# Kernel tuning notes

Measured on AMD Instinct MI355X. Metric: run time of the kernel, lower is better.

The kernel has to match this reference:

```python
import jax, jax.numpy as jnp
import numpy as np

B, T, N = 256, 512, 128
GO, EOS = 1, 2  # mead-baseline Offsets
NEG = -10000.0


def setup_inputs() -> dict:
    key = jax.random.key(0)
    k1, k2, k3 = jax.random.split(key, 3)
    unaries = jax.random.normal(k1, (B, T, N), dtype=jnp.float32)
    # constraint mask: True where transition is INVALID (masked to -1e4)
    cmask = jax.random.bernoulli(k2, 0.3, (1, N, N))
    trans = jax.nn.log_softmax(
        jnp.where(cmask, jnp.float32(NEG), jnp.float32(0.0)), axis=1
    )  # [1, N, N], matches buffer construction in __init__
    lengths = jax.random.randint(k3, (B,), T // 2, T + 1).astype(jnp.int64)
    lengths = lengths.at[0].set(T)  # ensure max(lengths) == T
    return {"unaries": unaries, "trans": trans, "lengths": lengths}


def _viterbi(probv, trans, lengths, start_idx, end_idx):
    # probv: [T, B, N] log-probs; trans: [1, N, N]; lengths: [B]
    seq_len, batch, n_tags = probv.shape
    trans0 = trans[0]  # [N(cur), N(prev)]
    lengths = lengths.astype(jnp.int32)

    alphas = jnp.full((batch, n_tags), NEG, probv.dtype).at[:, start_idx].set(0.0)
    alphas = jax.nn.log_softmax(alphas, axis=-1)

    def step(alphas, xs):
        unary_t, i = xs  # [B, N], scalar
        ntv = alphas[:, None, :] + trans0[None]          # [B, N_cur, N_prev]
        bp = jnp.argmax(ntv, axis=2)                     # backpointers [B, N]
        new_alphas = jnp.max(ntv, axis=2) + unary_t      # [B, N]
        alphas = jnp.where((i < lengths)[:, None], new_alphas, alphas)
        return alphas, bp

    alphas, bps = jax.lax.scan(step, alphas, (probv, jnp.arange(seq_len)))

    terminal = alphas + trans0[end_idx][None, :]         # [B, N]
    path_score = jnp.max(terminal, axis=1)               # [B]
    best_tag = jnp.argmax(terminal, axis=1)              # [B]

    rev_len = seq_len - lengths - 1

    def back(btid, xs):
        bp, i = xs  # bp: [B, N]
        new = jnp.take_along_axis(bp, btid[:, None], axis=1)[:, 0]
        btid = jnp.where(i > rev_len, new, btid)
        return btid, btid

    _, ys = jax.lax.scan(back, best_tag, (bps[::-1], jnp.arange(seq_len)))
    full = jnp.concatenate([best_tag[None], ys], axis=0)  # [T+1, B]
    best_path = full[:seq_len][::-1]                       # [T, B]

    seq_mask = jnp.arange(seq_len)[:, None] < lengths[None, :]  # [T, B]
    best_path = jnp.where(seq_mask, best_path, 0)
    return best_path, path_score


def reference(unaries, trans, lengths):
    # constrained branch of TaggerGreedyDecoder.forward (batch_first=True)
    probv = jax.nn.log_softmax(jnp.swapaxes(unaries, 0, 1), axis=-1)  # [T,B,N]
    preds_tb, scores = _viterbi(probv, trans, lengths, GO, EOS)
    return jnp.swapaxes(preds_tb, 0, 1), scores  # ([B,T], [B])
```

## Files before the change

### kernel.cpp

```cpp
#include <hip/hip_runtime.h>

#define BB 256
#define TT 512
#define NN 128
#define GO_IDX 1
#define EOS_IDX 2
#define TSPLIT 368
#define NEGV (-10000.0f)
#define ASLOT(x) ((x) + (((x) >> 5) << 2))

#define STEP_BARRIER() asm volatile("s_waitcnt lgkmcnt(0)\n\ts_barrier" ::: "memory")

typedef float f32x2 __attribute__((ext_vector_type(2)));

__device__ __forceinline__ f32x2 pk_add(f32x2 a, f32x2 b) {
    f32x2 d;
    asm("v_pk_add_f32 %0, %1, %2" : "=v"(d) : "v"(a), "v"(b));
    return d;
}

__device__ __forceinline__ float dpp_xor1_f(float x) {
    return __int_as_float(__builtin_amdgcn_update_dpp(0, __float_as_int(x), 0xB1, 0xF, 0xF, true));
}
__device__ __forceinline__ float dpp_xor2_f(float x) {
    return __int_as_float(__builtin_amdgcn_update_dpp(0, __float_as_int(x), 0x4E, 0xF, 0xF, true));
}
__device__ __forceinline__ int dpp_xor1_i(int x) {
    return __builtin_amdgcn_update_dpp(0, x, 0xB1, 0xF, 0xF, true);
}
__device__ __forceinline__ int dpp_xor2_i(int x) {
    return __builtin_amdgcn_update_dpp(0, x, 0x4E, 0xF, 0xF, true);
}

template <int USE_WS>
__global__ __launch_bounds__(512, 2) void viterbi_kernel(
    float* __restrict__ u,
    const float* __restrict__ trans,
    const int*   __restrict__ lengths_raw,
    float* __restrict__ out,
    unsigned char* __restrict__ ws)
{
    __shared__ unsigned char bps[(TSPLIT - 1) * NN];
    __shared__ __align__(16) float prob[2][16][NN];
    __shared__ __align__(16) float alpha[2][144];
    __shared__ float fin_v[2];
    __shared__ int   fin_i[2];

    const int tid  = threadIdx.x;
    const int b    = blockIdx.x;
    const int wave = tid >> 6;
    const int lane = tid & 63;
    const int q    = tid & 3;
    const int cur  = tid >> 2;
    const int hw   = tid >> 5;
    const int l32  = tid & 31;

    int len;
    {
        int probe = lengths_raw[1];
        len = (probe == 0) ? lengths_raw[2 * b] : lengths_raw[b];
    }

    float* pb = u + (size_t)b * TT * NN;
    const float4* pb4 = (const float4*)pb;
    unsigned char* spb = USE_WS ? (ws + (size_t)b * ((TT - TSPLIT) * NN)) : (unsigned char*)pb;

    f32x2 tr2[16];
    {
        const float4* t4 = (const float4*)(trans + cur * NN + q * 32);
#pragma unroll
        for (int i = 0; i < 8; ++i) {
            float4 v = t4[i];
            f32x2 lo; lo.x = v.x; lo.y = v.y;
            f32x2 hi; hi.x = v.z; hi.y = v.w;
            tr2[2 * i]     = lo;
            tr2[2 * i + 1] = hi;
        }
    }

    if (tid < NN) alpha[0][ASLOT(tid)] = (tid == GO_IDX) ? 0.0f : NEGV;

    auto normrow = [&](float4 v, float* dstrow) {
        float m = fmaxf(fmaxf(v.x, v.y), fmaxf(v.z, v.w));
#pragma unroll
        for (int off = 16; off; off >>= 1) m = fmaxf(m, __shfl_xor(m, off, 64));
        float s = expf(v.x - m) + expf(v.y - m) + expf(v.z - m) + expf(v.w - m);
#pragma unroll
        for (int off = 16; off; off >>= 1) s += __shfl_xor(s, off, 64);
        float ls = logf(s);
        ((float4*)dstrow)[l32] =
            make_float4((v.x - m) - ls, (v.y - m) - ls, (v.z - m) - ls, (v.w - m) - ls);
    };

    float4 R = pb4[hw * 32 + l32];
    normrow(R, &prob[0][hw][0]);
    R = pb4[(16 + hw) * 32 + l32];
    __syncthreads();

    const int nG = (len + 15) >> 4;
    for (int g = 0; g < nG; ++g) {
        const int tb = g << 4;
        normrow(R, &prob[(g + 1) & 1][hw][0]);
        {
            int rr = tb + 32 + hw;
            if (rr > TT - 1) rr = TT - 1;
            R = pb4[rr * 32 + l32];
        }
#pragma unroll 4
        for (int k = 0; k < 16; ++k) {
            const int t = tb + k;
            if (t < len) {
                const float Pv = prob[g & 1][k][cur];
                const float* ra = alpha[t & 1];
                float*       wa = alpha[(t & 1) ^ 1];
                const float4* a4 = (const float4*)(ra + q * 36);
                float bv[4]; int bi4[4];
#pragma unroll
                for (int c = 0; c < 4; ++c) {
                    float4 a0 = a4[c * 2], a1 = a4[c * 2 + 1];
                    f32x2 p0; p0.x = a0.x; p0.y = a0.y;
                    f32x2 p1; p1.x = a0.z; p1.y = a0.w;
                    f32x2 p2; p2.x = a1.x; p2.y = a1.y;
                    f32x2 p3; p3.x = a1.z; p3.y = a1.w;
                    f32x2 s0 = pk_add(p0, tr2[c * 4 + 0]);
                    f32x2 s1 = pk_add(p1, tr2[c * 4 + 1]);
                    f32x2 s2 = pk_add(p2, tr2[c * 4 + 2]);
                    f32x2 s3 = pk_add(p3, tr2[c * 4 + 3]);
                    const int base = c * 8;
                    bv[c] = s0.x; bi4[c] = base + 0;
                    float x;
                    x = s0.y; if (x > bv[c]) { bv[c] = x; bi4[c] = base + 1; }
                    x = s1.x; if (x > bv[c]) { bv[c] = x; bi4[c] = base + 2; }
                    x = s1.y; if (x > bv[c]) { bv[c] = x; bi4[c] = base + 3; }
                    x = s2.x; if (x > bv[c]) { bv[c] = x; bi4[c] = base + 4; }
                    x = s2.y; if (x > bv[c]) { bv[c] = x; bi4[c] = base + 5; }
                    x = s3.x; if (x > bv[c]) { bv[c] = x; bi4[c] = base + 6; }
                    x = s3.y; if (x > bv[c]) { bv[c] = x; bi4[c] = base + 7; }
                }
                float best = bv[0]; int bp = bi4[0];
#pragma unroll
                for (int c = 1; c < 4; ++c) { if (bv[c] > best) { best = bv[c]; bp = bi4[c]; } }
                bp += q * 32;

                float v1 = dpp_xor1_f(best);
                bool  t1 = (q & 1) ? (v1 >= best) : (v1 > best);
                float m1 = t1 ? v1 : best;
                float v2 = dpp_xor2_f(m1);
                bool  t2 = (q & 2) ? (v2 >= m1) : (v2 > m1);
                float M  = t2 ? v2 : m1;

                if (q == 0) wa[ASLOT(cur)] = M + Pv;

                int b1 = dpp_xor1_i(bp);
                int p1i = t1 ? b1 : bp;
                int b2 = dpp_xor2_i(p1i);
                int BP = t2 ? b2 : p1i;

                if (q == 0 && t >= 1) {
                    if (t < TSPLIT) bps[(t - 1) * NN + cur] = (unsigned char)BP;
                    else if (USE_WS) spb[(t - TSPLIT) * NN + cur] = (unsigned char)BP;
                    else             spb[(size_t)t * 512 + cur] = (unsigned char)BP;
                }
                STEP_BARRIER();
            }
        }
    }

    __threadfence();

    if (tid < NN) {
        float v = alpha[len & 1][ASLOT(tid)] + trans[EOS_IDX * NN + tid];
        int idx = tid;
#pragma unroll
        for (int off = 32; off; off >>= 1) {
            float ov = __shfl_xor(v, off, 64);
            int   oi = __shfl_xor(idx, off, 64);
            if (ov > v || (ov == v && oi < idx)) { v = ov; idx = oi; }
        }
        if (lane == 0) { fin_v[wave] = v; fin_i[wave] = idx; }
    }
    __syncthreads();

    const int lenU = __builtin_amdgcn_readfirstlane(len);

    for (int t = lenU + tid; t < TT; t += 512) out[(size_t)b * TT + t] = 0.0f;

    {
        unsigned int* cache = (unsigned int*)&prob[0][0][0];
        const volatile unsigned int* src = (const volatile unsigned int*)spb;
        for (int i = tid; i < 128 * 32; i += 512) {
            if (USE_WS) cache[i] = src[(size_t)(i >> 5) * 32 + (i & 31)];
            else        cache[i] = src[(size_t)(TSPLIT + (i >> 5)) * 128 + (i & 31)];
        }
    }
    __syncthreads();

    float sc; int T0;
    {
        float v0 = fin_v[0], v1 = fin_v[1];
        int   i0 = fin_i[0], i1 = fin_i[1];
        if (v1 > v0) { sc = v1; T0 = i1; }
        else         { sc = v0; T0 = i0; }
    }
    if (tid == 0) {
        out[(size_t)BB * TT + b] = sc;
        out[(size_t)b * TT + (lenU - 1)] = (float)T0;
    }

    const unsigned char* cacheb = (const unsigned char*)&prob[0][0][0];
    unsigned char* lt   = (unsigned char*)&alpha[0][0];
    unsigned char* Harr = lt + 1024;

    const int s  = wave;
    const int A  = lenU - 1 - 64 * s;
    const int h0 = lane;
    const int h1 = 64 + lane;
    const int Jmax = (A < 64) ? A : 64;

    unsigned int rec0[16], rec1[16];
#pragma unroll
    for (int i = 0; i < 16; ++i) { rec0[i] = 0u; rec1[i] = 0u; }

    int c0 = h0, c1 = h1;
#pragma unroll
    for (int j = 1; j <= 64; ++j) {
        if (j <= Jmax) {
            const int x = A - j + 1;
            int n0, n1;
            if (x < TSPLIT) {
                n0 = bps[(x - 1) * NN + c0];
                n1 = bps[(x - 1) * NN + c1];
            } else if (x < TSPLIT + 128) {
                n0 = cacheb[(x - TSPLIT) * NN + c0];
                n1 = cacheb[(x - TSPLIT) * NN + c1];
            } else {
                if (USE_WS) {
                    n0 = ((const volatile unsigned char*)spb)[(size_t)(x - TSPLIT) * NN + c0];
                    n1 = ((const volatile unsigned char*)spb)[(size_t)(x - TSPLIT) * NN + c1];
                } else {
                    n0 = ((const volatile unsigned char*)spb)[(size_t)x * 512 + c0];
                    n1 = ((const volatile unsigned char*)spb)[(size_t)x * 512 + c1];
                }
            }
            c0 = n0; c1 = n1;
            rec0[(j - 1) >> 2] |= (unsigned int)c0 << (((j - 1) & 3) * 8);
            rec1[(j - 1) >> 2] |= (unsigned int)c1 << (((j - 1) & 3) * 8);
        }
    }
    if (A >= 65) {
        lt[s * NN + h0] = (unsigned char)c0;
        lt[s * NN + h1] = (unsigned char)c1;
    }
    __syncthreads();

    if (tid == 0) {
        int H = T0;
        Harr[0] = (unsigned char)H;
#pragma unroll
        for (int ss = 1; ss < 8; ++ss) {
            if (lenU - 1 - 64 * ss >= 1) {
                H = lt[(ss - 1) * NN + H];
                Harr[ss] = (unsigned char)H;
            }
        }
    }
    __syncthreads();

    if (A >= 1) {
        const int Hs = Harr[s];
        if (h0 == Hs) {
#pragma unroll
            for (int j = 1; j <= 64; ++j)
                if (j <= Jmax)
                    out[(size_t)b * TT + (A - j)] =
                        (float)((rec0[(j - 1) >> 2] >> (((j - 1) & 3) * 8)) & 255u);
        }
        if (h1 == Hs) {
#pragma unroll
            for (int j = 1; j <= 64; ++j)
                if (j <= Jmax)
                    out[(size_t)b * TT + (A - j)] =
                        (float)((rec1[(j - 1) >> 2] >> (((j - 1) & 3) * 8)) & 255u);
        }
    }
}

extern "C" void kernel_launch(void* const* d_in, const int* in_sizes, int n_in,
                              void* d_out, int out_size, void* d_ws, size_t ws_size,
                              hipStream_t stream) {
    float*       unaries = (float*)d_in[0];
    const float* trans   = (const float*)d_in[1];
    const int*   lengths = (const int*)d_in[2];
    float* out = (float*)d_out;
    unsigned char* ws = (unsigned char*)d_ws;

    const size_t need = (size_t)BB * (TT - TSPLIT) * NN;
    if (ws != nullptr && ws_size >= need) {
        hipLaunchKernelGGL(HIP_KERNEL_NAME(viterbi_kernel<1>), dim3(BB), dim3(512), 0, stream,
                           unaries, trans, lengths, out, ws);
    } else {
        hipLaunchKernelGGL(HIP_KERNEL_NAME(viterbi_kernel<0>), dim3(BB), dim3(512), 0, stream,
                           unaries, trans, lengths, out, ws);
    }
}
```

Baseline: 499.0 us.

## Split Viterbi recurrence into max-only critical group and lagged backpointer group

```diff
diff --git a/kernel.cpp b/kernel.cpp
--- a/kernel.cpp
+++ b/kernel.cpp
@@ -5,7 +5,8 @@
 #define NN 128
 #define GO_IDX 1
 #define EOS_IDX 2
-#define TSPLIT 368
+#define TSPLIT 360
+#define LAG 2
 #define NEGV (-10000.0f)
 #define ASLOT(x) ((x) + (((x) >> 5) << 2))
 
@@ -33,7 +34,7 @@
 }
 
 template <int USE_WS>
-__global__ __launch_bounds__(512, 2) void viterbi_kernel(
+__global__ __launch_bounds__(1024) void viterbi_kernel(
     float* __restrict__ u,
     const float* __restrict__ trans,
     const int*   __restrict__ lengths_raw,
@@ -42,17 +43,19 @@
 {
     __shared__ unsigned char bps[(TSPLIT - 1) * NN];
     __shared__ __align__(16) float prob[2][16][NN];
-    __shared__ __align__(16) float alpha[2][144];
+    __shared__ __align__(16) float ring[4][144];
     __shared__ float fin_v[2];
     __shared__ int   fin_i[2];
 
     const int tid  = threadIdx.x;
     const int b    = blockIdx.x;
-    const int wave = tid >> 6;
+    const int grp  = tid >> 9;
+    const int lt   = tid & 511;
+    const int wv   = lt >> 6;
     const int lane = tid & 63;
-    const int q    = tid & 3;
-    const int cur  = tid >> 2;
-    const int hw   = tid >> 5;
+    const int q    = lt & 3;
+    const int cur  = lt >> 2;
+    const int hw   = lt >> 5;
     const int l32  = tid & 31;
 
     int len;
@@ -78,7 +81,7 @@
         }
     }
 
-    if (tid < NN) alpha[0][ASLOT(tid)] = (tid == GO_IDX) ? 0.0f : NEGV;
+    if (tid < NN) ring[0][ASLOT(tid)] = (tid == GO_IDX) ? 0.0f : NEGV;
 
     auto normrow = [&](float4 v, float* dstrow) {
         float m = fmaxf(fmaxf(v.x, v.y), fmaxf(v.z, v.w));
@@ -92,16 +95,22 @@
             make_float4((v.x - m) - ls, (v.y - m) - ls, (v.z - m) - ls, (v.w - m) - ls);
     };
 
-    float4 R = pb4[hw * 32 + l32];
-    normrow(R, &prob[0][hw][0]);
-    R = pb4[(16 + hw) * 32 + l32];
-    __syncthreads();
-
-    const int nG = (len + 15) >> 4;
+    float4 R;
+    if (grp == 1) {
+        R = pb4[hw * 32 + l32];
+        normrow(R, &prob[0][hw][0]);
+        R = pb4[(16 + hw) * 32 + l32];
+    }
+    __syncthreads();
+
+    if (grp == 0) __builtin_amdgcn_s_setprio(1);
+
+    const int lenP = len + LAG;
+    const int nG = (lenP + 15) >> 4;
     for (int g = 0; g < nG; ++g) {
         const int tb = g << 4;
-        normrow(R, &prob[(g + 1) & 1][hw][0]);
-        {
+        if (grp == 1) {
+            normrow(R, &prob[(g + 1) & 1][hw][0]);
             int rr = tb + 32 + hw;
             if (rr > TT - 1) rr = TT - 1;
             R = pb4[rr * 32 + l32];
@@ -109,67 +118,92 @@
 #pragma unroll 4
         for (int k = 0; k < 16; ++k) {
             const int t = tb + k;
-            if (t < len) {
-                const float Pv = prob[g & 1][k][cur];
-                const float* ra = alpha[t & 1];
-                float*       wa = alpha[(t & 1) ^ 1];
-                const float4* a4 = (const float4*)(ra + q * 36);
-                float bv[4]; int bi4[4];
-#pragma unroll
-                for (int c = 0; c < 4; ++c) {
-                    float4 a0 = a4[c * 2], a1 = a4[c * 2 + 1];
-                    f32x2 p0; p0.x = a0.x; p0.y = a0.y;
-                    f32x2 p1; p1.x = a0.z; p1.y = a0.w;
-                    f32x2 p2; p2.x = a1.x; p2.y = a1.y;
-                    f32x2 p3; p3.x = a1.z; p3.y = a1.w;
-                    f32x2 s0 = pk_add(p0, tr2[c * 4 + 0]);
-                    f32x2 s1 = pk_add(p1, tr2[c * 4 + 1]);
-                    f32x2 s2 = pk_add(p2, tr2[c * 4 + 2]);
-                    f32x2 s3 = pk_add(p3, tr2[c * 4 + 3]);
-                    const int base = c * 8;
-                    bv[c] = s0.x; bi4[c] = base + 0;
-                    float x;
-                    x = s0.y; if (x > bv[c]) { bv[c] = x; bi4[c] = base + 1; }
-                    x = s1.x; if (x > bv[c]) { bv[c] = x; bi4[c] = base + 2; }
-                    x = s1.y; if (x > bv[c]) { bv[c] = x; bi4[c] = base + 3; }
-                    x = s2.x; if (x > bv[c]) { bv[c] = x; bi4[c] = base + 4; }
-                    x = s2.y; if (x > bv[c]) { bv[c] = x; bi4[c] = base + 5; }
-                    x = s3.x; if (x > bv[c]) { bv[c] = x; bi4[c] = base + 6; }
-                    x = s3.y; if (x > bv[c]) { bv[c] = x; bi4[c] = base + 7; }
-                }
-                float best = bv[0]; int bp = bi4[0];
-#pragma unroll
-                for (int c = 1; c < 4; ++c) { if (bv[c] > best) { best = bv[c]; bp = bi4[c]; } }
-                bp += q * 32;
-
-                float v1 = dpp_xor1_f(best);
-                bool  t1 = (q & 1) ? (v1 >= best) : (v1 > best);
-                float m1 = t1 ? v1 : best;
-                float v2 = dpp_xor2_f(m1);
-                bool  t2 = (q & 2) ? (v2 >= m1) : (v2 > m1);
-                float M  = t2 ? v2 : m1;
-
-                if (q == 0) wa[ASLOT(cur)] = M + Pv;
-
-                int b1 = dpp_xor1_i(bp);
-                int p1i = t1 ? b1 : bp;
-                int b2 = dpp_xor2_i(p1i);
-                int BP = t2 ? b2 : p1i;
-
-                if (q == 0 && t >= 1) {
-                    if (t < TSPLIT) bps[(t - 1) * NN + cur] = (unsigned char)BP;
-                    else if (USE_WS) spb[(t - TSPLIT) * NN + cur] = (unsigned char)BP;
-                    else             spb[(size_t)t * 512 + cur] = (unsigned char)BP;
+            if (t < lenP) {
+                if (grp == 0) {
+                    if (t < len) {
+                        const float Pv = prob[g & 1][k][cur];
+                        const float* ra = ring[t & 3];
+                        float*       wa = ring[(t + 1) & 3];
+                        const float4* a4 = (const float4*)(ra + q * 36);
+                        float bm[4];
+#pragma unroll
+                        for (int c = 0; c < 4; ++c) {
+                            float4 a0 = a4[c * 2], a1 = a4[c * 2 + 1];
+                            f32x2 p0; p0.x = a0.x; p0.y = a0.y;
+                            f32x2 p1; p1.x = a0.z; p1.y = a0.w;
+                            f32x2 p2; p2.x = a1.x; p2.y = a1.y;
+                            f32x2 p3; p3.x = a1.z; p3.y = a1.w;
+                            f32x2 s0 = pk_add(p0, tr2[c * 4 + 0]);
+                            f32x2 s1 = pk_add(p1, tr2[c * 4 + 1]);
+                            f32x2 s2 = pk_add(p2, tr2[c * 4 + 2]);
+                            f32x2 s3 = pk_add(p3, tr2[c * 4 + 3]);
+                            float m01 = fmaxf(fmaxf(s0.x, s0.y), fmaxf(s1.x, s1.y));
+                            float m23 = fmaxf(fmaxf(s2.x, s2.y), fmaxf(s3.x, s3.y));
+                            bm[c] = fmaxf(m01, m23);
+                        }
+                        float M = fmaxf(fmaxf(bm[0], bm[1]), fmaxf(bm[2], bm[3]));
+                        M = fmaxf(M, dpp_xor1_f(M));
+                        M = fmaxf(M, dpp_xor2_f(M));
+                        if (q == 0) wa[ASLOT(cur)] = M + Pv;
+                    }
+                } else {
+                    const int tbp = t - LAG;
+                    if (tbp >= 1 && tbp < len) {
+                        const float* ra = ring[tbp & 3];
+                        const float4* a4 = (const float4*)(ra + q * 36);
+                        float bv[4]; int bi4[4];
+#pragma unroll
+                        for (int c = 0; c < 4; ++c) {
+                            float4 a0 = a4[c * 2], a1 = a4[c * 2 + 1];
+                            f32x2 p0; p0.x = a0.x; p0.y = a0.y;
+                            f32x2 p1; p1.x = a0.z; p1.y = a0.w;
+                            f32x2 p2; p2.x = a1.x; p2.y = a1.y;
+                            f32x2 p3; p3.x = a1.z; p3.y = a1.w;
+                            f32x2 s0 = pk_add(p0, tr2[c * 4 + 0]);
+                            f32x2 s1 = pk_add(p1, tr2[c * 4 + 1]);
+                            f32x2 s2 = pk_add(p2, tr2[c * 4 + 2]);
+                            f32x2 s3 = pk_add(p3, tr2[c * 4 + 3]);
+                            const int base = c * 8;
+                            bv[c] = s0.x; bi4[c] = base + 0;
+                            float x;
+                            x = s0.y; if (x > bv[c]) { bv[c] = x; bi4[c] = base + 1; }
+                            x = s1.x; if (x > bv[c]) { bv[c] = x; bi4[c] = base + 2; }
+                            x = s1.y; if (x > bv[c]) { bv[c] = x; bi4[c] = base + 3; }
+                            x = s2.x; if (x > bv[c]) { bv[c] = x; bi4[c] = base + 4; }
+                            x = s2.y; if (x > bv[c]) { bv[c] = x; bi4[c] = base + 5; }
+                            x = s3.x; if (x > bv[c]) { bv[c] = x; bi4[c] = base + 6; }
+                            x = s3.y; if (x > bv[c]) { bv[c] = x; bi4[c] = base + 7; }
+                        }
+                        float best = bv[0]; int bp = bi4[0];
+#pragma unroll
+                        for (int c = 1; c < 4; ++c) { if (bv[c] > best) { best = bv[c]; bp = bi4[c]; } }
+                        bp += q * 32;
+
+                        float v1 = dpp_xor1_f(best); int b1 = dpp_xor1_i(bp);
+                        bool  t1 = (q & 1) ? (v1 >= best) : (v1 > best);
+                        float m1 = t1 ? v1 : best;   int p1i = t1 ? b1 : bp;
+                        float v2 = dpp_xor2_f(m1);   int b2 = dpp_xor2_i(p1i);
+                        bool  t2 = (q & 2) ? (v2 >= m1) : (v2 > m1);
+                        int BP = t2 ? b2 : p1i;
+
+                        if (q == 0) {
+                            if (tbp < TSPLIT) bps[(tbp - 1) * NN + cur] = (unsigned char)BP;
+                            else if (USE_WS)  spb[(tbp - TSPLIT) * NN + cur] = (unsigned char)BP;
+                            else              spb[(size_t)tbp * 512 + cur] = (unsigned char)BP;
+                        }
+                    }
                 }
                 STEP_BARRIER();
             }
         }
     }
 
+    if (grp == 0) __builtin_amdgcn_s_setprio(0);
+
     __threadfence();
 
     if (tid < NN) {
-        float v = alpha[len & 1][ASLOT(tid)] + trans[EOS_IDX * NN + tid];
+        float v = ring[len & 3][ASLOT(tid)] + trans[EOS_IDX * NN + tid];
         int idx = tid;
 #pragma unroll
         for (int off = 32; off; off >>= 1) {
@@ -177,18 +211,18 @@
             int   oi = __shfl_xor(idx, off, 64);
             if (ov > v || (ov == v && oi < idx)) { v = ov; idx = oi; }
         }
-        if (lane == 0) { fin_v[wave] = v; fin_i[wave] = idx; }
+        if (lane == 0) { fin_v[wv] = v; fin_i[wv] = idx; }
     }
     __syncthreads();
 
     const int lenU = __builtin_amdgcn_readfirstlane(len);
 
-    for (int t = lenU + tid; t < TT; t += 512) out[(size_t)b * TT + t] = 0.0f;
+    for (int t = lenU + tid; t < TT; t += 1024) out[(size_t)b * TT + t] = 0.0f;
 
     {
         unsigned int* cache = (unsigned int*)&prob[0][0][0];
         const volatile unsigned int* src = (const volatile unsigned int*)spb;
-        for (int i = tid; i < 128 * 32; i += 512) {
+        for (int i = tid; i < 128 * 32; i += 1024) {
             if (USE_WS) cache[i] = src[(size_t)(i >> 5) * 32 + (i & 31)];
             else        cache[i] = src[(size_t)(TSPLIT + (i >> 5)) * 128 + (i & 31)];
         }
@@ -208,48 +242,50 @@
     }
 
     const unsigned char* cacheb = (const unsigned char*)&prob[0][0][0];
-    unsigned char* lt   = (unsigned char*)&alpha[0][0];
-    unsigned char* Harr = lt + 1024;
-
-    const int s  = wave;
+    unsigned char* lt_tab = (unsigned char*)&ring[0][0];
+    unsigned char* Harr   = lt_tab + 1024;
+
+    const int s  = wv;
     const int A  = lenU - 1 - 64 * s;
     const int h0 = lane;
     const int h1 = 64 + lane;
     const int Jmax = (A < 64) ? A : 64;
 
     unsigned int rec0[16], rec1[16];
-#pragma unroll
-    for (int i = 0; i < 16; ++i) { rec0[i] = 0u; rec1[i] = 0u; }
-
-    int c0 = h0, c1 = h1;
-#pragma unroll
-    for (int j = 1; j <= 64; ++j) {
-        if (j <= Jmax) {
-            const int x = A - j + 1;
-            int n0, n1;
-            if (x < TSPLIT) {
-                n0 = bps[(x - 1) * NN + c0];
-                n1 = bps[(x - 1) * NN + c1];
-            } else if (x < TSPLIT + 128) {
-                n0 = cacheb[(x - TSPLIT) * NN + c0];
-                n1 = cacheb[(x - TSPLIT) * NN + c1];
-            } else {
-                if (USE_WS) {
-                    n0 = ((const volatile unsigned char*)spb)[(size_t)(x - TSPLIT) * NN + c0];
-                    n1 = ((const volatile unsigned char*)spb)[(size_t)(x - TSPLIT) * NN + c1];
+    if (grp == 0) {
+#pragma unroll
+        for (int i = 0; i < 16; ++i) { rec0[i] = 0u; rec1[i] = 0u; }
+
+        int c0 = h0, c1 = h1;
+#pragma unroll
+        for (int j = 1; j <= 64; ++j) {
+            if (j <= Jmax) {
+                const int x = A - j + 1;
+                int n0, n1;
+                if (x < TSPLIT) {
+                    n0 = bps[(x - 1) * NN + c0];
+                    n1 = bps[(x - 1) * NN + c1];
+                } else if (x < TSPLIT + 128) {
+                    n0 = cacheb[(x - TSPLIT) * NN + c0];
+                    n1 = cacheb[(x - TSPLIT) * NN + c1];
                 } else {
-                    n0 = ((const volatile unsigned char*)spb)[(size_t)x * 512 + c0];
-                    n1 = ((const volatile unsigned char*)spb)[(size_t)x * 512 + c1];
+                    if (USE_WS) {
+                        n0 = ((const volatile unsigned char*)spb)[(size_t)(x - TSPLIT) * NN + c0];
+                        n1 = ((const volatile unsigned char*)spb)[(size_t)(x - TSPLIT) * NN + c1];
+                    } else {
+                        n0 = ((const volatile unsigned char*)spb)[(size_t)x * 512 + c0];
+                        n1 = ((const volatile unsigned char*)spb)[(size_t)x * 512 + c1];
+                    }
                 }
+                c0 = n0; c1 = n1;
+                rec0[(j - 1) >> 2] |= (unsigned int)c0 << (((j - 1) & 3) * 8);
+                rec1[(j - 1) >> 2] |= (unsigned int)c1 << (((j - 1) & 3) * 8);
             }
-            c0 = n0; c1 = n1;
-            rec0[(j - 1) >> 2] |= (unsigned int)c0 << (((j - 1) & 3) * 8);
-            rec1[(j - 1) >> 2] |= (unsigned int)c1 << (((j - 1) & 3) * 8);
-        }
-    }
-    if (A >= 65) {
-        lt[s * NN + h0] = (unsigned char)c0;
-        lt[s * NN + h1] = (unsigned char)c1;
+        }
+        if (A >= 65) {
+            lt_tab[s * NN + h0] = (unsigned char)c0;
+            lt_tab[s * NN + h1] = (unsigned char)c1;
+        }
     }
     __syncthreads();
 
@@ -259,14 +295,14 @@
 #pragma unroll
         for (int ss = 1; ss < 8; ++ss) {
             if (lenU - 1 - 64 * ss >= 1) {
-                H = lt[(ss - 1) * NN + H];
+                H = lt_tab[(ss - 1) * NN + H];
                 Harr[ss] = (unsigned char)H;
             }
         }
     }
     __syncthreads();
 
-    if (A >= 1) {
+    if (grp == 0 && A >= 1) {
         const int Hs = Harr[s];
         if (h0 == Hs) {
 #pragma unroll
@@ -296,10 +332,10 @@
 
     const size_t need = (size_t)BB * (TT - TSPLIT) * NN;
     if (ws != nullptr && ws_size >= need) {
-        hipLaunchKernelGGL(HIP_KERNEL_NAME(viterbi_kernel<1>), dim3(BB), dim3(512), 0, stream,
+        hipLaunchKernelGGL(HIP_KERNEL_NAME(viterbi_kernel<1>), dim3(BB), dim3(1024), 0, stream,
                            unaries, trans, lengths, out, ws);
     } else {
-        hipLaunchKernelGGL(HIP_KERNEL_NAME(viterbi_kernel<0>), dim3(BB), dim3(512), 0, stream,
+        hipLaunchKernelGGL(HIP_KERNEL_NAME(viterbi_kernel<0>), dim3(BB), dim3(1024), 0, stream,
                            unaries, trans, lengths, out, ws);
     }
 }
```

Result: slower. 575.6 us (+15.3%).
